# Kernel tuning notes

Hardware: AMD Instinct MI355X
Metric: run time of the kernel (lower is better)

The kernel has to match this reference:

```python
import jax, jax.numpy as jnp
import numpy as np

D_MODEL = 1024
NHEAD = 16
HEAD_DIM = D_MODEL // NHEAD  # 64
Q_STRIDE = 2
KV_STRIDE = 1
ROPE_BASE = 10000.0


def _rope_tables(positions):
    # positions: [L] int -> cos/sin [L, HEAD_DIM]
    half = HEAD_DIM // 2
    inv_freq = 1.0 / (ROPE_BASE ** (jnp.arange(half, dtype=jnp.float32) / half))
    freqs = positions.astype(jnp.float32)[:, None] * inv_freq[None, :]  # [L, half]
    emb = jnp.concatenate([freqs, freqs], axis=-1)  # [L, HEAD_DIM]
    return jnp.cos(emb), jnp.sin(emb)


def _rotate_half(x):
    half = x.shape[-1] // 2
    return jnp.concatenate([-x[..., half:], x[..., :half]], axis=-1)


def _apply_rope(x, cos, sin):
    # x: [B, H, L, D]; cos/sin: [L, D] broadcast over B, H
    return x * cos + _rotate_half(x) * sin


def setup_inputs() -> dict:
    key = jax.random.key(0)
    ks = jax.random.split(key, 10)
    B, S, K = 4, 1024, 2048
    s = 0.02
    return {
        "query": jax.random.normal(ks[0], (B, S, D_MODEL), jnp.float32),
        "kv": jax.random.normal(ks[1], (B, K, D_MODEL), jnp.float32),
        "q_w": jax.random.normal(ks[2], (D_MODEL, D_MODEL), jnp.float32) * s,
        "q_b": jax.random.normal(ks[3], (D_MODEL,), jnp.float32) * s,
        "k_w": jax.random.normal(ks[4], (D_MODEL, D_MODEL), jnp.float32) * s,
        "k_b": jax.random.normal(ks[5], (D_MODEL,), jnp.float32) * s,
        "v_w": jax.random.normal(ks[6], (D_MODEL, D_MODEL), jnp.float32) * s,
        "v_b": jax.random.normal(ks[7], (D_MODEL,), jnp.float32) * s,
        "out_w": jax.random.normal(ks[8], (D_MODEL, D_MODEL), jnp.float32) * s,
        "out_b": jax.random.normal(ks[9], (D_MODEL,), jnp.float32) * s,
    }


def reference(query, kv, q_w, q_b, k_w, k_b, v_w, v_b, out_w, out_b):
    B, S, _ = query.shape
    K = kv.shape[1]
    # Projections (torch Linear: x @ W^T + b), reshape to [B, H, L, D]
    q = (query @ q_w.T + q_b).reshape(B, S, NHEAD, HEAD_DIM).transpose(0, 2, 1, 3)
    k = (kv @ k_w.T + k_b).reshape(B, K, NHEAD, HEAD_DIM).transpose(0, 2, 1, 3)
    v = (kv @ v_w.T + v_b).reshape(B, K, NHEAD, HEAD_DIM).transpose(0, 2, 1, 3)
    # RoPE at strided original frame positions
    q_cos, q_sin = _rope_tables(jnp.arange(S) * Q_STRIDE)
    k_cos, k_sin = _rope_tables(jnp.arange(K) * KV_STRIDE)
    q = _apply_rope(q, q_cos, q_sin)
    k = _apply_rope(k, k_cos, k_sin)
    scale = 1.0 / np.sqrt(HEAD_DIM).astype(np.float32)
    attn = jnp.einsum('bhsd,bhkd->bhsk', q, k) * scale  # [B, H, S, K]
    attn = jax.nn.softmax(attn, axis=-1)
    out = jnp.einsum('bhsk,bhkd->bhsd', attn, v)
    out = out.transpose(0, 2, 1, 3).reshape(B, S, D_MODEL)
    return out @ out_w.T + out_b
```

## Files before the change

### kernel.cpp

```cpp
#include <hip/hip_runtime.h>
#include <hip/hip_bf16.h>

#define D_MODEL 1024
#define NHEAD   16
#define HD      64
#define SQ      1024
#define SK      2048

typedef __attribute__((ext_vector_type(8))) short bh8;
typedef __attribute__((ext_vector_type(4))) float fx4;

#define QSCALE 0.1803368801111204f

__device__ __forceinline__ unsigned short f2bf(float f) {
  union { float f; unsigned u; } v; v.f = f;
  return (unsigned short)((v.u + 0x7FFFu + ((v.u >> 16) & 1u)) >> 16);
}

__device__ __forceinline__ float bf2f(unsigned short u) {
  union { unsigned u; float f; } v; v.u = ((unsigned)u) << 16; return v.f;
}

#define GLOAD_LDS16(gp, lp)                                                  \
  __builtin_amdgcn_global_load_lds(                                         \
      (const __attribute__((address_space(1))) unsigned int*)(gp),          \
      (__attribute__((address_space(3))) unsigned int*)(lp), 16, 0, 0)

__global__ __launch_bounds__(256) void cvt_kernel(
    const float* __restrict__ q, const float* __restrict__ kv,
    const float* __restrict__ qw, const float* __restrict__ kw,
    const float* __restrict__ vw, const float* __restrict__ ow,
    unsigned short* __restrict__ qx, unsigned short* __restrict__ kvx,
    unsigned short* __restrict__ qwx, unsigned short* __restrict__ kwx,
    unsigned short* __restrict__ vwx, unsigned short* __restrict__ owx)
{
  const int idx = blockIdx.x * 256 + threadIdx.x;
  const float* src; unsigned short* dst; size_t off;
  if (idx < 524288)        { src = q;  dst = qx;  off = idx; }
  else if (idx < 1572864)  { src = kv; dst = kvx; off = idx - 524288; }
  else {
    const int w = idx - 1572864; const int sel = w >> 17; off = w & 131071;
    src = sel == 0 ? qw : sel == 1 ? kw : sel == 2 ? vw : ow;
    dst = sel == 0 ? qwx : sel == 1 ? kwx : sel == 2 ? vwx : owx;
  }
  const float4 a = ((const float4*)src)[off * 2];
  const float4 b = ((const float4*)src)[off * 2 + 1];
  bh8 r;
  r[0] = (short)f2bf(a.x); r[1] = (short)f2bf(a.y);
  r[2] = (short)f2bf(a.z); r[3] = (short)f2bf(a.w);
  r[4] = (short)f2bf(b.x); r[5] = (short)f2bf(b.y);
  r[6] = (short)f2bf(b.z); r[7] = (short)f2bf(b.w);
  *(bh8*)(dst + off * 8) = r;
}

__global__ __launch_bounds__(256) void qkv_kernel(
    const unsigned short* __restrict__ qx, const unsigned short* __restrict__ kvx,
    const unsigned short* __restrict__ qw, const unsigned short* __restrict__ kw,
    const unsigned short* __restrict__ vw,
    const float* __restrict__ qb, const float* __restrict__ kb,
    const float* __restrict__ vb,
    unsigned short* __restrict__ outq, unsigned short* __restrict__ outk,
    unsigned short* __restrict__ outv)
{
  __shared__ unsigned short Alds[2][4096];
  __shared__ unsigned short Blds[2][4096];

  const int t = threadIdx.x;
  const int lane = t & 63, w = t >> 6;
  const int lr = lane & 15, g = lane >> 4, kl = g * 8;
  const int bid = (blockIdx.x & 7) * 160 + (blockIdx.x >> 3);
  const bool isQ = bid >= 1024;
  int bx, by;
  if (isQ) { const int tq = bid - 1024; bx = tq >> 5; by = tq & 31; }
  else     { bx = bid >> 6; by = bid & 63; }
  const int row0 = by * 128;
  const int colB = bx * 128;
  const int wrow = (w >> 1) * 64;
  const int wcol = (w & 1) * 64;

  const unsigned short* X = isQ ? qx : kvx;
  const unsigned short* Wsrc; const float* bias; int colW; bool isK = false;
  if (isQ)              { Wsrc = qw; bias = qb; colW = colB; }
  else if (colB < 1024) { Wsrc = kw; bias = kb; colW = colB; isK = true; }
  else                  { Wsrc = vw; bias = vb; colW = colB - 1024; }

  const int srow = t >> 2, schunk = (t & 3) * 8;

#define STAGE_P(k0_, bi_) do {                                                        \
    GLOAD_LDS16(X + (size_t)(row0 + srow) * 1024 + (k0_) + schunk,                    \
                &Alds[bi_][t * 8]);                                                   \
    GLOAD_LDS16(X + (size_t)(row0 + 64 + srow) * 1024 + (k0_) + schunk,               \
                &Alds[bi_][2048 + t * 8]);                                            \
    GLOAD_LDS16(Wsrc + (size_t)(colW + srow) * 1024 + (k0_) + schunk,                 \
                &Blds[bi_][t * 8]);                                                   \
    GLOAD_LDS16(Wsrc + (size_t)(colW + 64 + srow) * 1024 + (k0_) + schunk,            \
                &Blds[bi_][2048 + t * 8]);                                            \
  } while (0)

  fx4 acc[4][4] = {};
  STAGE_P(0, 0);
  for (int k0 = 0; k0 < 1024; k0 += 32) {
    const int cur = (k0 >> 5) & 1;
    __syncthreads();
    if (k0 + 32 < 1024) STAGE_P(k0 + 32, cur ^ 1);

    bh8 af[4], bf[4];
#pragma unroll
    for (int mi = 0; mi < 4; ++mi)
      af[mi] = *(const bh8*)&Alds[cur][(wrow + mi * 16 + lr) * 32 + kl];
#pragma unroll
    for (int ni = 0; ni < 4; ++ni)
      bf[ni] = *(const bh8*)&Blds[cur][(wcol + ni * 16 + lr) * 32 + kl];
    __builtin_amdgcn_s_setprio(1);
#pragma unroll
    for (int mi = 0; mi < 4; ++mi)
#pragma unroll
      for (int ni = 0; ni < 4; ++ni)
        acc[mi][ni] = __builtin_amdgcn_mfma_f32_16x16x32_bf16(af[mi], bf[ni], acc[mi][ni], 0, 0, 0);
    __builtin_amdgcn_s_setprio(0);
  }

  float bv[4];
#pragma unroll
  for (int ni = 0; ni < 4; ++ni) bv[ni] = bias[colW + wcol + ni * 16 + lr];
#pragma unroll
  for (int mi = 0; mi < 4; ++mi)
#pragma unroll
    for (int ni = 0; ni < 4; ++ni)
#pragma unroll
      for (int j = 0; j < 4; ++j) acc[mi][ni][j] += bv[ni];

  const int LMASK = isQ ? 1023 : 2047;
  if (isQ || isK) {
    const float c0 = 0.41524101186092029f;
    const float invf0 = exp2f(-(float)lr * c0);
    const float invf1 = exp2f(-(float)(16 + lr) * c0);
#pragma unroll
    for (int mi = 0; mi < 4; ++mi)
#pragma unroll
      for (int j = 0; j < 4; ++j) {
        const int rg = row0 + wrow + mi * 16 + 4 * g + j;
        const int s = rg & LMASK;
        const float pos = (float)(isQ ? 2 * s : s);
#pragma unroll
        for (int ni = 0; ni < 2; ++ni) {
          float sn, cs;
          __sincosf(pos * (ni == 0 ? invf0 : invf1), &sn, &cs);
          const float x1 = acc[mi][ni][j], x2 = acc[mi][ni + 2][j];
          acc[mi][ni][j]     = x1 * cs - x2 * sn;
          acc[mi][ni + 2][j] = x2 * cs + x1 * sn;
        }
      }
  }

  const int h = (colW + wcol) >> 6;
#pragma unroll
  for (int mi = 0; mi < 4; ++mi)
#pragma unroll
    for (int j = 0; j < 4; ++j) {
      const int rg = row0 + wrow + mi * 16 + 4 * g + j;
      const int bb = isQ ? (rg >> 10) : (rg >> 11);
      const int s = rg & LMASK;
#pragma unroll
      for (int ni = 0; ni < 4; ++ni) {
        const int d = ni * 16 + lr;
        if (isQ) {
          outq[(((size_t)(bb * 16 + h)) * SQ + s) * 64 + d] = f2bf(acc[mi][ni][j] * QSCALE);
        } else {
          const size_t base = ((size_t)(bb * 16 + h)) * (SK * 64);
          if (isK)
            outk[base + (s >> 4) * 1024 + (d >> 5) * 512 + ((d >> 3) & 3) * 128 + (s & 15) * 8 + (d & 7)]
                = f2bf(acc[mi][ni][j]);
          else
            outv[base + (s >> 5) * 2048 + (d >> 4) * 512 + ((s >> 3) & 3) * 128 + (d & 15) * 8 + (s & 7)]
                = f2bf(acc[mi][ni][j]);
        }
      }
    }
}

__global__ __launch_bounds__(256) void oproj_kernel(
    const unsigned short* __restrict__ A, const unsigned short* __restrict__ W,
    const float* __restrict__ bias, float* __restrict__ out)
{
  __shared__ unsigned short Alds[2][4096];
  __shared__ unsigned short Blds[2][4096];

  const int t = threadIdx.x;
  const int lane = t & 63, w = t >> 6;
  const int lr = lane & 15, g = lane >> 4, kl = g * 8;
  const int row0 = blockIdx.y * 128;
  const int colB = blockIdx.x * 128;
  const int wrow = (w >> 1) * 64;
  const int wcol = (w & 1) * 64;
  const int srow = t >> 2, schunk = (t & 3) * 8;

#define STAGE_O(k0_, bi_) do {                                                        \
    GLOAD_LDS16(A + (size_t)(row0 + srow) * 1024 + (k0_) + schunk,                    \
                &Alds[bi_][t * 8]);                                                   \
    GLOAD_LDS16(A + (size_t)(row0 + 64 + srow) * 1024 + (k0_) + schunk,               \
                &Alds[bi_][2048 + t * 8]);                                            \
    GLOAD_LDS16(W + (size_t)(colB + srow) * 1024 + (k0_) + schunk,                    \
                &Blds[bi_][t * 8]);                                                   \
    GLOAD_LDS16(W + (size_t)(colB + 64 + srow) * 1024 + (k0_) + schunk,               \
                &Blds[bi_][2048 + t * 8]);                                            \
  } while (0)

  fx4 acc[4][4] = {};
  STAGE_O(0, 0);
  for (int k0 = 0; k0 < 1024; k0 += 32) {
    const int cur = (k0 >> 5) & 1;
    __syncthreads();
    if (k0 + 32 < 1024) STAGE_O(k0 + 32, cur ^ 1);

    bh8 af[4], bf[4];
#pragma unroll
    for (int mi = 0; mi < 4; ++mi)
      af[mi] = *(const bh8*)&Alds[cur][(wrow + mi * 16 + lr) * 32 + kl];
#pragma unroll
    for (int ni = 0; ni < 4; ++ni)
      bf[ni] = *(const bh8*)&Blds[cur][(wcol + ni * 16 + lr) * 32 + kl];
    __builtin_amdgcn_s_setprio(1);
#pragma unroll
    for (int mi = 0; mi < 4; ++mi)
#pragma unroll
      for (int ni = 0; ni < 4; ++ni)
        acc[mi][ni] = __builtin_amdgcn_mfma_f32_16x16x32_bf16(af[mi], bf[ni], acc[mi][ni], 0, 0, 0);
    __builtin_amdgcn_s_setprio(0);
  }

  float bv[4];
#pragma unroll
  for (int ni = 0; ni < 4; ++ni) bv[ni] = bias[colB + wcol + ni * 16 + lr];
#pragma unroll
  for (int mi = 0; mi < 4; ++mi)
#pragma unroll
    for (int j = 0; j < 4; ++j) {
      const int rg = row0 + wrow + mi * 16 + 4 * g + j;
#pragma unroll
      for (int ni = 0; ni < 4; ++ni)
        out[(size_t)rg * 1024 + colB + wcol + ni * 16 + lr] = acc[mi][ni][j] + bv[ni];
    }
}

__global__ __launch_bounds__(256, 4) void attn_kernel(
    const unsigned short* __restrict__ Qr, const unsigned short* __restrict__ Kt,
    const unsigned short* __restrict__ Vt, unsigned short* __restrict__ O)
{
  __shared__ __align__(16) unsigned short smem[4 * 2304];
  __shared__ float llds[4][32];

  const int lane = threadIdx.x & 63;
  const int w = threadIdx.x >> 6;
  const int lr = lane & 15, g = lane >> 4, kl = g * 8;
  const int bid = blockIdx.x;
  const int swz = (bid & 7) * 256 + (bid >> 3);
  const int bh = swz >> 5;
  const int q0 = (swz & 31) * 32;
  const int b = bh >> 4, h = bh & 15;

  unsigned short* p_lds = smem + w * 2304;

  const unsigned short* Qp = Qr + (size_t)bh * SQ * HD;
  const unsigned short* Kp = Kt + (size_t)bh * SK * HD;
  const unsigned short* Vp = Vt + (size_t)bh * SK * HD;

  bh8 qf[2][2];
#pragma unroll
  for (int mi = 0; mi < 2; ++mi)
#pragma unroll
    for (int kk = 0; kk < 2; ++kk)
      qf[mi][kk] = *(const bh8*)(Qp + (size_t)(q0 + mi * 16 + lr) * 64 + kk * 32 + kl);

  bh8 ones;
#pragma unroll
  for (int i = 0; i < 8; ++i) ones[i] = (short)0x3F80;

  fx4 oacc[2][4] = {};
  fx4 lacc[2] = {};

  for (int t = 0; t < 8; ++t) {
    fx4 sacc[2][4] = {};
#pragma unroll
    for (int kk = 0; kk < 2; ++kk) {
      bh8 kf[4];
#pragma unroll
      for (int ni = 0; ni < 4; ++ni)
        kf[ni] = *(const bh8*)(Kp + (size_t)(w * 32 + t * 4 + ni) * 1024 + kk * 512 + g * 128 + lr * 8);
      __builtin_amdgcn_s_setprio(1);
#pragma unroll
      for (int mi = 0; mi < 2; ++mi)
#pragma unroll
        for (int ni = 0; ni < 4; ++ni)
          sacc[mi][ni] = __builtin_amdgcn_mfma_f32_16x16x32_bf16(qf[mi][kk], kf[ni], sacc[mi][ni], 0, 0, 0);
      __builtin_amdgcn_s_setprio(0);
    }

    asm volatile("s_waitcnt lgkmcnt(0)" ::: "memory");
    __builtin_amdgcn_sched_barrier(0);

#pragma unroll
    for (int mi = 0; mi < 2; ++mi)
#pragma unroll
      for (int ni = 0; ni < 4; ++ni) {
        float p0, p1, p2, p3;
        asm("v_exp_f32 %0, %1" : "=v"(p0) : "v"(sacc[mi][ni][0]));
        asm("v_exp_f32 %0, %1" : "=v"(p1) : "v"(sacc[mi][ni][1]));
        asm("v_exp_f32 %0, %1" : "=v"(p2) : "v"(sacc[mi][ni][2]));
        asm("v_exp_f32 %0, %1" : "=v"(p3) : "v"(sacc[mi][ni][3]));
        unsigned lo, hi;
        asm("v_cvt_pk_bf16_f32 %0, %1, %2" : "=v"(lo) : "v"(p0), "v"(p1));
        asm("v_cvt_pk_bf16_f32 %0, %1, %2" : "=v"(hi) : "v"(p2), "v"(p3));
        unsigned short* base = &p_lds[(mi * 16 + 4 * g) * 68 + ni * 16 + lr];
        base[0]   = (unsigned short)lo;
        base[68]  = (unsigned short)(lo >> 16);
        base[136] = (unsigned short)hi;
        base[204] = (unsigned short)(hi >> 16);
      }

    asm volatile("s_waitcnt lgkmcnt(0)" ::: "memory");
    __builtin_amdgcn_sched_barrier(0);

#pragma unroll
    for (int kk = 0; kk < 2; ++kk) {
      bh8 pa[2], vb[4];
#pragma unroll
      for (int mi = 0; mi < 2; ++mi) {
        const unsigned short* pp = &p_lds[(mi * 16 + lr) * 68 + kk * 32 + kl];
        const short4 a = *(const short4*)pp;
        const short4 c = *(const short4*)(pp + 4);
        pa[mi][0] = a.x; pa[mi][1] = a.y; pa[mi][2] = a.z; pa[mi][3] = a.w;
        pa[mi][4] = c.x; pa[mi][5] = c.y; pa[mi][6] = c.z; pa[mi][7] = c.w;
      }
#pragma unroll
      for (int ni = 0; ni < 4; ++ni)
        vb[ni] = *(const bh8*)(Vp + (size_t)(w * 16 + t * 2 + kk) * 2048 + ni * 512 + g * 128 + lr * 8);
      __builtin_amdgcn_s_setprio(1);
#pragma unroll
      for (int mi = 0; mi < 2; ++mi) {
#pragma unroll
        for (int ni = 0; ni < 4; ++ni)
          oacc[mi][ni] = __builtin_amdgcn_mfma_f32_16x16x32_bf16(pa[mi], vb[ni], oacc[mi][ni], 0, 0, 0);
        lacc[mi] = __builtin_amdgcn_mfma_f32_16x16x32_bf16(pa[mi], ones, lacc[mi], 0, 0, 0);
      }
      __builtin_amdgcn_s_setprio(0);
    }
  }

  if (lr == 0) {
#pragma unroll
    for (int mi = 0; mi < 2; ++mi)
#pragma unroll
      for (int j = 0; j < 4; ++j)
        llds[w][mi * 16 + 4 * g + j] = lacc[mi][j];
  }

  asm volatile("s_waitcnt lgkmcnt(0)" ::: "memory");
  __builtin_amdgcn_sched_barrier(0);
  unsigned short* opart = smem + w * 2304;
#pragma unroll
  for (int mi = 0; mi < 2; ++mi)
#pragma unroll
    for (int j = 0; j < 4; ++j) {
      const int row = mi * 16 + 4 * g + j;
#pragma unroll
      for (int ni = 0; ni < 4; ++ni)
        opart[row * 72 + ni * 16 + lr] = f2bf(oacc[mi][ni][j]);
    }
  __syncthreads();

  const int row = threadIdx.x >> 3;
  const int d0 = (threadIdx.x & 7) * 8;
  float a8[8] = {};
#pragma unroll
  for (int ww = 0; ww < 4; ++ww) {
    const bh8 v = *(const bh8*)(smem + ww * 2304 + row * 72 + d0);
#pragma unroll
    for (int i = 0; i < 8; ++i) a8[i] += bf2f((unsigned short)v[i]);
  }
  const float inv = 1.0f / (llds[0][row] + llds[1][row] + llds[2][row] + llds[3][row]);
  bh8 r;
#pragma unroll
  for (int i = 0; i < 8; ++i) r[i] = (short)f2bf(a8[i] * inv);
  *(bh8*)&O[((size_t)(b * SQ + q0 + row)) * D_MODEL + h * 64 + d0] = r;
}

extern "C" void kernel_launch(void* const* d_in, const int* in_sizes, int n_in,
                              void* d_out, int out_size, void* d_ws, size_t ws_size,
                              hipStream_t stream) {
  (void)in_sizes; (void)n_in; (void)out_size; (void)ws_size;
  const float* query = (const float*)d_in[0];
  const float* kv    = (const float*)d_in[1];
  const float* q_w   = (const float*)d_in[2];
  const float* q_b   = (const float*)d_in[3];
  const float* k_w   = (const float*)d_in[4];
  const float* k_b   = (const float*)d_in[5];
  const float* v_w   = (const float*)d_in[6];
  const float* v_b   = (const float*)d_in[7];
  const float* out_w = (const float*)d_in[8];
  const float* out_b = (const float*)d_in[9];
  float* out = (float*)d_out;

  unsigned short* ws = (unsigned short*)d_ws;
  unsigned short* qx     = ws;
  unsigned short* kvx    = ws + ((size_t)4  << 20);
  unsigned short* qwx    = ws + ((size_t)12 << 20);
  unsigned short* kwx    = ws + ((size_t)13 << 20);
  unsigned short* vwx    = ws + ((size_t)14 << 20);
  unsigned short* owx    = ws + ((size_t)15 << 20);
  unsigned short* q_rope = ws + ((size_t)16 << 20);
  unsigned short* k_t    = ws + ((size_t)20 << 20);
  unsigned short* v_t    = ws + ((size_t)28 << 20);
  unsigned short* attn_o = qx;

  hipLaunchKernelGGL(cvt_kernel, dim3(8192), dim3(256), 0, stream,
                     query, kv, q_w, k_w, v_w, out_w, qx, kvx, qwx, kwx, vwx, owx);
  hipLaunchKernelGGL(qkv_kernel, dim3(1280), dim3(256), 0, stream,
                     qx, kvx, qwx, kwx, vwx, q_b, k_b, v_b, q_rope, k_t, v_t);
  hipLaunchKernelGGL(attn_kernel, dim3(2048), dim3(256), 0, stream,
                     q_rope, k_t, v_t, attn_o);
  hipLaunchKernelGGL(oproj_kernel, dim3(8, 32), dim3(256), 0, stream,
                     attn_o, owx, out_b, out);
}
```

Measured before the change: 172.5 us.

## Deepen GEMM prefetch to 4-stage pipeline, shrink oproj tile, remap block order

Both projection GEMMs move from a double-buffered LDS loop with __syncthreads to a 4-buffer ring that prefetches three k-tiles ahead, using explicit vmcnt waits and a raw s_barrier. The aim is to hide global-load latency behind more in-flight loads. The output projection tile shrinks from 128x128 to 64x128 with a 1D grid of 512 blocks, giving more blocks to fill the CUs. The qkv block index swizzle is replaced by a row-major mapping. Costs are larger LDS footprint (lower occupancy in qkv) and possibly worse L2 locality from the changed block ordering.

```diff
diff --git a/kernel.cpp b/kernel.cpp
--- a/kernel.cpp
+++ b/kernel.cpp
@@ -62,17 +62,17 @@
     unsigned short* __restrict__ outq, unsigned short* __restrict__ outk,
     unsigned short* __restrict__ outv)
 {
-  __shared__ unsigned short Alds[2][4096];
-  __shared__ unsigned short Blds[2][4096];
+  __shared__ unsigned short Alds[4][4096];
+  __shared__ unsigned short Blds[4][4096];
 
   const int t = threadIdx.x;
   const int lane = t & 63, w = t >> 6;
   const int lr = lane & 15, g = lane >> 4, kl = g * 8;
-  const int bid = (blockIdx.x & 7) * 160 + (blockIdx.x >> 3);
+  const int bid = blockIdx.x;
   const bool isQ = bid >= 1024;
   int bx, by;
-  if (isQ) { const int tq = bid - 1024; bx = tq >> 5; by = tq & 31; }
-  else     { bx = bid >> 6; by = bid & 63; }
+  if (isQ) { const int tq = bid - 1024; bx = tq & 7; by = tq >> 3; }
+  else     { bx = bid & 15; by = bid >> 4; }
   const int row0 = by * 128;
   const int colB = bx * 128;
   const int wrow = (w >> 1) * 64;
@@ -99,10 +99,17 @@
 
   fx4 acc[4][4] = {};
   STAGE_P(0, 0);
-  for (int k0 = 0; k0 < 1024; k0 += 32) {
-    const int cur = (k0 >> 5) & 1;
-    __syncthreads();
-    if (k0 + 32 < 1024) STAGE_P(k0 + 32, cur ^ 1);
+  STAGE_P(32, 1);
+  STAGE_P(64, 2);
+  for (int kt = 0; kt < 32; ++kt) {
+    const int cur = kt & 3;
+    if (kt < 30)       asm volatile("s_waitcnt vmcnt(8)" ::: "memory");
+    else if (kt == 30) asm volatile("s_waitcnt vmcnt(4)" ::: "memory");
+    else               asm volatile("s_waitcnt vmcnt(0)" ::: "memory");
+    __builtin_amdgcn_sched_barrier(0);
+    __builtin_amdgcn_s_barrier();
+    __builtin_amdgcn_sched_barrier(0);
+    if (kt <= 28) STAGE_P((kt + 3) * 32, (kt + 3) & 3);
 
     bh8 af[4], bf[4];
 #pragma unroll
@@ -183,46 +190,54 @@
     const unsigned short* __restrict__ A, const unsigned short* __restrict__ W,
     const float* __restrict__ bias, float* __restrict__ out)
 {
-  __shared__ unsigned short Alds[2][4096];
-  __shared__ unsigned short Blds[2][4096];
+  __shared__ unsigned short Alds[4][2048];
+  __shared__ unsigned short Blds[4][4096];
 
   const int t = threadIdx.x;
   const int lane = t & 63, w = t >> 6;
   const int lr = lane & 15, g = lane >> 4, kl = g * 8;
-  const int row0 = blockIdx.y * 128;
-  const int colB = blockIdx.x * 128;
-  const int wrow = (w >> 1) * 64;
+  const int bid = blockIdx.x;
+  const int bx = bid & 7, by = bid >> 3;
+  const int row0 = by * 64;
+  const int colB = bx * 128;
+  const int wrow = (w >> 1) * 32;
   const int wcol = (w & 1) * 64;
-  const int srow = t >> 2, schunk = (t & 3) * 8;
+  const int srowA = t >> 2, schunkA = (t & 3) * 8;
+  const int srowB = t >> 2, schunkB = (t & 3) * 8;
 
 #define STAGE_O(k0_, bi_) do {                                                        \
-    GLOAD_LDS16(A + (size_t)(row0 + srow) * 1024 + (k0_) + schunk,                    \
+    GLOAD_LDS16(A + (size_t)(row0 + srowA) * 1024 + (k0_) + schunkA,                  \
                 &Alds[bi_][t * 8]);                                                   \
-    GLOAD_LDS16(A + (size_t)(row0 + 64 + srow) * 1024 + (k0_) + schunk,               \
-                &Alds[bi_][2048 + t * 8]);                                            \
-    GLOAD_LDS16(W + (size_t)(colB + srow) * 1024 + (k0_) + schunk,                    \
+    GLOAD_LDS16(W + (size_t)(colB + srowB) * 1024 + (k0_) + schunkB,                  \
                 &Blds[bi_][t * 8]);                                                   \
-    GLOAD_LDS16(W + (size_t)(colB + 64 + srow) * 1024 + (k0_) + schunk,               \
+    GLOAD_LDS16(W + (size_t)(colB + 64 + srowB) * 1024 + (k0_) + schunkB,             \
                 &Blds[bi_][2048 + t * 8]);                                            \
   } while (0)
 
-  fx4 acc[4][4] = {};
+  fx4 acc[2][4] = {};
   STAGE_O(0, 0);
-  for (int k0 = 0; k0 < 1024; k0 += 32) {
-    const int cur = (k0 >> 5) & 1;
-    __syncthreads();
-    if (k0 + 32 < 1024) STAGE_O(k0 + 32, cur ^ 1);
-
-    bh8 af[4], bf[4];
-#pragma unroll
-    for (int mi = 0; mi < 4; ++mi)
+  STAGE_O(32, 1);
+  STAGE_O(64, 2);
+  for (int kt = 0; kt < 32; ++kt) {
+    const int cur = kt & 3;
+    if (kt < 30)       asm volatile("s_waitcnt vmcnt(6)" ::: "memory");
+    else if (kt == 30) asm volatile("s_waitcnt vmcnt(3)" ::: "memory");
+    else               asm volatile("s_waitcnt vmcnt(0)" ::: "memory");
+    __builtin_amdgcn_sched_barrier(0);
+    __builtin_amdgcn_s_barrier();
+    __builtin_amdgcn_sched_barrier(0);
+    if (kt <= 28) STAGE_O((kt + 3) * 32, (kt + 3) & 3);
+
+    bh8 af[2], bf[4];
+#pragma unroll
+    for (int mi = 0; mi < 2; ++mi)
       af[mi] = *(const bh8*)&Alds[cur][(wrow + mi * 16 + lr) * 32 + kl];
 #pragma unroll
     for (int ni = 0; ni < 4; ++ni)
       bf[ni] = *(const bh8*)&Blds[cur][(wcol + ni * 16 + lr) * 32 + kl];
     __builtin_amdgcn_s_setprio(1);
 #pragma unroll
-    for (int mi = 0; mi < 4; ++mi)
+    for (int mi = 0; mi < 2; ++mi)
 #pragma unroll
       for (int ni = 0; ni < 4; ++ni)
         acc[mi][ni] = __builtin_amdgcn_mfma_f32_16x16x32_bf16(af[mi], bf[ni], acc[mi][ni], 0, 0, 0);
@@ -233,7 +248,7 @@
 #pragma unroll
   for (int ni = 0; ni < 4; ++ni) bv[ni] = bias[colB + wcol + ni * 16 + lr];
 #pragma unroll
-  for (int mi = 0; mi < 4; ++mi)
+  for (int mi = 0; mi < 2; ++mi)
 #pragma unroll
     for (int j = 0; j < 4; ++j) {
       const int rg = row0 + wrow + mi * 16 + 4 * g + j;
@@ -419,6 +434,6 @@
                      qx, kvx, qwx, kwx, vwx, q_b, k_b, v_b, q_rope, k_t, v_t);
   hipLaunchKernelGGL(attn_kernel, dim3(2048), dim3(256), 0, stream,
                      q_rope, k_t, v_t, attn_o);
-  hipLaunchKernelGGL(oproj_kernel, dim3(8, 32), dim3(256), 0, stream,
+  hipLaunchKernelGGL(oproj_kernel, dim3(512), dim3(256), 0, stream,
                      attn_o, owx, out_b, out);
 }
```

Result: no change. 171.2 us (-0.8%).

## Shrink projection GEMM tiles to 64x128 and drop LDS double buffering

Applied to the files above, without the earlier changes.

The QKV and output-projection GEMMs move from 128x128 tiles to 64x128 tiles, doubling the block count (2560 and 512) so more CUs stay busy. The double-buffered LDS prefetch is replaced by a single buffer with load, sync, compute, and the XCD-swizzled block mapping is removed in favour of a linear one. Smaller tiles lower per-block register and LDS use and raise occupancy. In exchange, A-tile reuse drops, global traffic per FLOP rises, and global-load latency is no longer hidden behind MFMA work.

```diff
diff --git a/kernel.cpp b/kernel.cpp
--- a/kernel.cpp
+++ b/kernel.cpp
@@ -62,20 +62,20 @@
     unsigned short* __restrict__ outq, unsigned short* __restrict__ outk,
     unsigned short* __restrict__ outv)
 {
-  __shared__ unsigned short Alds[2][4096];
-  __shared__ unsigned short Blds[2][4096];
+  __shared__ unsigned short Alds[2048];
+  __shared__ unsigned short Blds[4096];
 
   const int t = threadIdx.x;
   const int lane = t & 63, w = t >> 6;
   const int lr = lane & 15, g = lane >> 4, kl = g * 8;
-  const int bid = (blockIdx.x & 7) * 160 + (blockIdx.x >> 3);
-  const bool isQ = bid >= 1024;
+  const int bid = blockIdx.x;
+  const bool isQ = bid >= 2048;
   int bx, by;
-  if (isQ) { const int tq = bid - 1024; bx = tq >> 5; by = tq & 31; }
-  else     { bx = bid >> 6; by = bid & 63; }
-  const int row0 = by * 128;
+  if (isQ) { const int tq = bid - 2048; bx = tq & 7; by = tq >> 3; }
+  else     { bx = bid & 15; by = bid >> 4; }
+  const int row0 = by * 64;
   const int colB = bx * 128;
-  const int wrow = (w >> 1) * 64;
+  const int wrow = (w >> 1) * 32;
   const int wcol = (w & 1) * 64;
 
   const unsigned short* X = isQ ? qx : kvx;
@@ -86,34 +86,29 @@
 
   const int srow = t >> 2, schunk = (t & 3) * 8;
 
-#define STAGE_P(k0_, bi_) do {                                                        \
-    GLOAD_LDS16(X + (size_t)(row0 + srow) * 1024 + (k0_) + schunk,                    \
-                &Alds[bi_][t * 8]);                                                   \
-    GLOAD_LDS16(X + (size_t)(row0 + 64 + srow) * 1024 + (k0_) + schunk,               \
-                &Alds[bi_][2048 + t * 8]);                                            \
-    GLOAD_LDS16(Wsrc + (size_t)(colW + srow) * 1024 + (k0_) + schunk,                 \
-                &Blds[bi_][t * 8]);                                                   \
+#define STAGE_P(k0_) do {                                                             \
+    GLOAD_LDS16(X + (size_t)(row0 + srow) * 1024 + (k0_) + schunk, &Alds[t * 8]);     \
+    GLOAD_LDS16(Wsrc + (size_t)(colW + srow) * 1024 + (k0_) + schunk, &Blds[t * 8]);  \
     GLOAD_LDS16(Wsrc + (size_t)(colW + 64 + srow) * 1024 + (k0_) + schunk,            \
-                &Blds[bi_][2048 + t * 8]);                                            \
+                &Blds[2048 + t * 8]);                                                 \
   } while (0)
 
-  fx4 acc[4][4] = {};
-  STAGE_P(0, 0);
+  fx4 acc[2][4] = {};
   for (int k0 = 0; k0 < 1024; k0 += 32) {
-    const int cur = (k0 >> 5) & 1;
     __syncthreads();
-    if (k0 + 32 < 1024) STAGE_P(k0 + 32, cur ^ 1);
-
-    bh8 af[4], bf[4];
-#pragma unroll
-    for (int mi = 0; mi < 4; ++mi)
-      af[mi] = *(const bh8*)&Alds[cur][(wrow + mi * 16 + lr) * 32 + kl];
+    STAGE_P(k0);
+    __syncthreads();
+
+    bh8 af[2], bf[4];
+#pragma unroll
+    for (int mi = 0; mi < 2; ++mi)
+      af[mi] = *(const bh8*)&Alds[(wrow + mi * 16 + lr) * 32 + kl];
 #pragma unroll
     for (int ni = 0; ni < 4; ++ni)
-      bf[ni] = *(const bh8*)&Blds[cur][(wcol + ni * 16 + lr) * 32 + kl];
+      bf[ni] = *(const bh8*)&Blds[(wcol + ni * 16 + lr) * 32 + kl];
     __builtin_amdgcn_s_setprio(1);
 #pragma unroll
-    for (int mi = 0; mi < 4; ++mi)
+    for (int mi = 0; mi < 2; ++mi)
 #pragma unroll
       for (int ni = 0; ni < 4; ++ni)
         acc[mi][ni] = __builtin_amdgcn_mfma_f32_16x16x32_bf16(af[mi], bf[ni], acc[mi][ni], 0, 0, 0);
@@ -124,7 +119,7 @@
 #pragma unroll
   for (int ni = 0; ni < 4; ++ni) bv[ni] = bias[colW + wcol + ni * 16 + lr];
 #pragma unroll
-  for (int mi = 0; mi < 4; ++mi)
+  for (int mi = 0; mi < 2; ++mi)
 #pragma unroll
     for (int ni = 0; ni < 4; ++ni)
 #pragma unroll
@@ -136,7 +131,7 @@
     const float invf0 = exp2f(-(float)lr * c0);
     const float invf1 = exp2f(-(float)(16 + lr) * c0);
 #pragma unroll
-    for (int mi = 0; mi < 4; ++mi)
+    for (int mi = 0; mi < 2; ++mi)
 #pragma unroll
       for (int j = 0; j < 4; ++j) {
         const int rg = row0 + wrow + mi * 16 + 4 * g + j;
@@ -155,7 +150,7 @@
 
   const int h = (colW + wcol) >> 6;
 #pragma unroll
-  for (int mi = 0; mi < 4; ++mi)
+  for (int mi = 0; mi < 2; ++mi)
 #pragma unroll
     for (int j = 0; j < 4; ++j) {
       const int rg = row0 + wrow + mi * 16 + 4 * g + j;
@@ -183,46 +178,43 @@
     const unsigned short* __restrict__ A, const unsigned short* __restrict__ W,
     const float* __restrict__ bias, float* __restrict__ out)
 {
-  __shared__ unsigned short Alds[2][4096];
-  __shared__ unsigned short Blds[2][4096];
+  __shared__ unsigned short Alds[2048];
+  __shared__ unsigned short Blds[4096];
 
   const int t = threadIdx.x;
   const int lane = t & 63, w = t >> 6;
   const int lr = lane & 15, g = lane >> 4, kl = g * 8;
-  const int row0 = blockIdx.y * 128;
-  const int colB = blockIdx.x * 128;
-  const int wrow = (w >> 1) * 64;
+  const int bid = blockIdx.x;
+  const int bx = bid & 7, by = bid >> 3;
+  const int row0 = by * 64;
+  const int colB = bx * 128;
+  const int wrow = (w >> 1) * 32;
   const int wcol = (w & 1) * 64;
   const int srow = t >> 2, schunk = (t & 3) * 8;
 
-#define STAGE_O(k0_, bi_) do {                                                        \
-    GLOAD_LDS16(A + (size_t)(row0 + srow) * 1024 + (k0_) + schunk,                    \
-                &Alds[bi_][t * 8]);                                                   \
-    GLOAD_LDS16(A + (size_t)(row0 + 64 + srow) * 1024 + (k0_) + schunk,               \
-                &Alds[bi_][2048 + t * 8]);                                            \
-    GLOAD_LDS16(W + (size_t)(colB + srow) * 1024 + (k0_) + schunk,                    \
-                &Blds[bi_][t * 8]);                                                   \
+#define STAGE_O(k0_) do {                                                             \
+    GLOAD_LDS16(A + (size_t)(row0 + srow) * 1024 + (k0_) + schunk, &Alds[t * 8]);     \
+    GLOAD_LDS16(W + (size_t)(colB + srow) * 1024 + (k0_) + schunk, &Blds[t * 8]);     \
     GLOAD_LDS16(W + (size_t)(colB + 64 + srow) * 1024 + (k0_) + schunk,               \
-                &Blds[bi_][2048 + t * 8]);                                            \
+                &Blds[2048 + t * 8]);                                                 \
   } while (0)
 
-  fx4 acc[4][4] = {};
-  STAGE_O(0, 0);
+  fx4 acc[2][4] = {};
   for (int k0 = 0; k0 < 1024; k0 += 32) {
-    const int cur = (k0 >> 5) & 1;
     __syncthreads();
-    if (k0 + 32 < 1024) STAGE_O(k0 + 32, cur ^ 1);
-
-    bh8 af[4], bf[4];
-#pragma unroll
-    for (int mi = 0; mi < 4; ++mi)
-      af[mi] = *(const bh8*)&Alds[cur][(wrow + mi * 16 + lr) * 32 + kl];
+    STAGE_O(k0);
+    __syncthreads();
+
+    bh8 af[2], bf[4];
+#pragma unroll
+    for (int mi = 0; mi < 2; ++mi)
+      af[mi] = *(const bh8*)&Alds[(wrow + mi * 16 + lr) * 32 + kl];
 #pragma unroll
     for (int ni = 0; ni < 4; ++ni)
-      bf[ni] = *(const bh8*)&Blds[cur][(wcol + ni * 16 + lr) * 32 + kl];
+      bf[ni] = *(const bh8*)&Blds[(wcol + ni * 16 + lr) * 32 + kl];
     __builtin_amdgcn_s_setprio(1);
 #pragma unroll
-    for (int mi = 0; mi < 4; ++mi)
+    for (int mi = 0; mi < 2; ++mi)
 #pragma unroll
       for (int ni = 0; ni < 4; ++ni)
         acc[mi][ni] = __builtin_amdgcn_mfma_f32_16x16x32_bf16(af[mi], bf[ni], acc[mi][ni], 0, 0, 0);
@@ -233,7 +225,7 @@
 #pragma unroll
   for (int ni = 0; ni < 4; ++ni) bv[ni] = bias[colB + wcol + ni * 16 + lr];
 #pragma unroll
-  for (int mi = 0; mi < 4; ++mi)
+  for (int mi = 0; mi < 2; ++mi)
 #pragma unroll
     for (int j = 0; j < 4; ++j) {
       const int rg = row0 + wrow + mi * 16 + 4 * g + j;
@@ -415,10 +407,10 @@
 
   hipLaunchKernelGGL(cvt_kernel, dim3(8192), dim3(256), 0, stream,
                      query, kv, q_w, k_w, v_w, out_w, qx, kvx, qwx, kwx, vwx, owx);
-  hipLaunchKernelGGL(qkv_kernel, dim3(1280), dim3(256), 0, stream,
+  hipLaunchKernelGGL(qkv_kernel, dim3(2560), dim3(256), 0, stream,
                      qx, kvx, qwx, kwx, vwx, q_b, k_b, v_b, q_rope, k_t, v_t);
   hipLaunchKernelGGL(attn_kernel, dim3(2048), dim3(256), 0, stream,
                      q_rope, k_t, v_t, attn_o);
-  hipLaunchKernelGGL(oproj_kernel, dim3(8, 32), dim3(256), 0, stream,
+  hipLaunchKernelGGL(oproj_kernel, dim3(512), dim3(256), 0, stream,
                      attn_o, owx, out_b, out);
 }
```

Result: faster. 167.5 us (-2.9%).
